# Kernel tuning notes

Measured on AMD Instinct MI355X. Metric: run time of the kernel, lower is better.

The kernel has to match this reference:

```python
import jax, jax.numpy as jnp
import numpy as np

N_E = 1024
E_DIM = 256
BETA = 0.25
PERSISTENCE = 0.1
B, T = 16, 1024


def setup_inputs() -> dict:
    key = jax.random.key(0)
    k1, k2 = jax.random.split(key)
    z = jax.random.normal(k1, (B, T, E_DIM), dtype=jnp.float32)
    # nn.Embedding(1+n_e, e_dim) init uniform(-1/n_e, 1/n_e)
    emb_weight = jax.random.uniform(k2, (N_E + 1, E_DIM), dtype=jnp.float32,
                                    minval=-1.0 / N_E, maxval=1.0 / N_E)
    return {"z": z, "emb_weight": emb_weight}


def _loss_contrast(z, ind, book):
    # z: (B,T,e), ind: (B,T) int, book: (n_e+1, e)
    z_q = book[ind]                                   # (B,T,e)
    loss_indices = jnp.sum((z - z_q) ** 2, axis=-1)   # (B,T)
    # ||z - book||^2 expanded to avoid the (B,T,n_e+1,e) intermediate
    z_sq = jnp.sum(z * z, axis=-1)                    # (B,T)
    b_sq = jnp.sum(book * book, axis=-1)              # (n_e+1,)
    cross = jnp.einsum('bte,ne->btn', z, book)        # (B,T,n_e+1)
    loss_all = z_sq[..., None] + b_sq[None, None, :] - 2.0 * cross
    lc = jnp.maximum(loss_indices[..., None] - loss_all + 1e-6 / N_E, 0.0)
    return jnp.mean(lc)


def _forward(z, emb_weight):
    zf = z.reshape(-1, E_DIM)
    d = (jnp.sum(zf * zf, axis=1, keepdims=True)
         + jnp.sum(emb_weight * emb_weight, axis=1)
         - 2.0 * (zf @ emb_weight.T)).reshape(B, T, N_E + 1)

    ind0 = jnp.clip(jnp.argmin(d[:, 0, :], axis=1), 0, N_E - 1)  # (B,)

    def step(carry, d_t):
        ind, coe = carry                              # (B,) int, (B,) f32
        d_here = jnp.take_along_axis(d_t, ind[:, None], axis=1)[:, 0]
        ind_next = jnp.minimum(ind + 1, N_E - 1)
        d_next = jnp.take_along_axis(d_t, ind_next[:, None], axis=1)[:, 0]
        stay = d_here <= d_next - coe
        ind_new = jnp.where(stay, ind, ind_next)
        coe_new = jnp.where(stay, coe + PERSISTENCE / N_E, 0.0)
        return (ind_new, coe_new), ind_new

    coe0 = jnp.zeros((B,), jnp.float32)
    _, inds = jax.lax.scan(step, (ind0, coe0), jnp.swapaxes(d[:, 1:, :], 0, 1))
    encoding_indices = jnp.concatenate([ind0[None, :], inds], axis=0).T  # (B,T)

    book_sg = jax.lax.stop_gradient(emb_weight)  # torch uses .data/.detach() everywhere
    z_q_raw = book_sg[encoding_indices]
    z_q = z + jax.lax.stop_gradient(z_q_raw - z)  # straight-through

    # non-legacy: beta * L(z, sg(book)) + L(sg(z), sg(book))
    loss = (BETA * _loss_contrast(z, encoding_indices, book_sg)
            + _loss_contrast(jax.lax.stop_gradient(z), encoding_indices, book_sg))

    v = jnp.max(encoding_indices) - jnp.min(encoding_indices)
    return z_q, loss, encoding_indices, v


def reference(z, emb_weight):
    return _forward(z, emb_weight)
```

## Files before the change

kernel.cpp:

```cpp
#include <hip/hip_runtime.h>

#define N_E   1024
#define EDIM  256
#define BB    16
#define TT    1024
#define NROW  (BB*TT)
#define NCOL  1025
#define NPAD  1152
#define PERS  (0.1f/1024.0f)
#define EPSC  (1e-6f/1024.0f)

#define OUT_LOSS 4194304
#define OUT_IDX  4194305
#define OUT_V    4210689

#define WS_ZB   0ull
#define WS_BBF  8388608ull
#define WS_BSQ  8978432ull
#define WS_E    8983552ull
#define WS_IND  84481024ull
#define WS_PART 84546560ull

typedef __attribute__((ext_vector_type(8))) short short8;
typedef __attribute__((ext_vector_type(4))) float floatx4;

__device__ __forceinline__ unsigned short f2bf(float f) {
    unsigned int u = __float_as_uint(f);
    u = (u + 0x7fffu + ((u >> 16) & 1u)) >> 16;
    return (unsigned short)u;
}

__device__ __forceinline__ float gload_f32(const float* p) {
    float r;
    asm volatile("global_load_dword %0, %1, off" : "=v"(r) : "v"(p));
    return r;
}

__global__ __launch_bounds__(256) void k0_prep(const float* __restrict__ z,
                                               const float* __restrict__ book,
                                               unsigned short* __restrict__ zb,
                                               unsigned short* __restrict__ bb,
                                               float* __restrict__ bsq) {
    int bx = blockIdx.x, tid = threadIdx.x;
    if (bx < 4096) {
        float4 v = ((const float4*)z)[bx * 256 + tid];
        size_t o = ((size_t)bx * 256 + tid) * 4;
        zb[o + 0] = f2bf(v.x); zb[o + 1] = f2bf(v.y);
        zb[o + 2] = f2bf(v.z); zb[o + 3] = f2bf(v.w);
    } else {
        int row = bx - 4096;
        float v = (row < NCOL) ? book[(size_t)row * EDIM + tid] : 0.0f;
        bb[(size_t)row * EDIM + tid] = f2bf(v);
        __shared__ float sd[256];
        sd[tid] = v * v;
        __syncthreads();
        for (int s = 128; s > 0; s >>= 1) { if (tid < s) sd[tid] += sd[tid + s]; __syncthreads(); }
        if (tid == 0) bsq[row] = sd[0];
    }
}

__global__ __launch_bounds__(256) void k1_gemm(const unsigned short* __restrict__ zb,
                                               const unsigned short* __restrict__ bb,
                                               const float* __restrict__ bsq,
                                               float* __restrict__ e) {
    int tid = threadIdx.x;
    int lane = tid & 63, w = tid >> 6;
    int mBase = blockIdx.x * 128 + (w >> 1) * 64;
    int nBase = blockIdx.y * 128 + (w & 1) * 64;
    int r = lane & 15, q = lane >> 4;

    floatx4 acc[4][4];
    #pragma unroll
    for (int i = 0; i < 4; i++)
        #pragma unroll
        for (int j = 0; j < 4; j++) acc[i][j] = (floatx4){0.f, 0.f, 0.f, 0.f};

    const short8* A = (const short8*)zb;
    const short8* Bm = (const short8*)bb;

    #pragma unroll
    for (int ks = 0; ks < 8; ks++) {
        int k8 = ks * 4 + q;
        short8 a[4], b[4];
        #pragma unroll
        for (int i = 0; i < 4; i++) a[i] = A[(size_t)(mBase + i * 16 + r) * 32 + k8];
        #pragma unroll
        for (int j = 0; j < 4; j++) b[j] = Bm[(size_t)(nBase + j * 16 + r) * 32 + k8];
        #pragma unroll
        for (int i = 0; i < 4; i++)
            #pragma unroll
            for (int j = 0; j < 4; j++)
                acc[i][j] = __builtin_amdgcn_mfma_f32_16x16x32_bf16(a[i], b[j], acc[i][j], 0, 0, 0);
    }

    float bsql[4];
    #pragma unroll
    for (int j = 0; j < 4; j++) bsql[j] = bsq[nBase + j * 16 + r];

    #pragma unroll
    for (int i = 0; i < 4; i++)
        #pragma unroll
        for (int rr = 0; rr < 4; rr++) {
            int m = mBase + i * 16 + q * 4 + rr;
            float* erow = e + (size_t)m * NPAD;
            #pragma unroll
            for (int j = 0; j < 4; j++)
                erow[nBase + j * 16 + r] = fmaf(-2.0f, acc[i][j][rr], bsql[j]);
        }
}


#define GCH 6

#define DECLW float A0_0, A0_1, A0_2, A1_0, A1_1, A1_2, \
                    A2_0, A2_1, A2_2, A3_0, A3_1, A3_2; \
              int q_0, q_1, q_2;

#define LDOP(S,k) { int _t = ti + 2*k + _g; _t = _t < 1024 ? _t : 1023; \
                    A##S##_##k = gload_f32(_pe + (size_t)_t * NPAD); }
#define LDSET0 LDOP(0,0) LDOP(0,1) LDOP(0,2)
#define LDSET1 LDOP(1,0) LDOP(1,1) LDOP(1,2)
#define LDSET2 LDOP(2,0) LDOP(2,1) LDOP(2,2)
#define LDSET3 LDOP(3,0) LDOP(3,1) LDOP(3,2)

#define QCOP(S,k) { float _bv = __shfl_down(A##S##_##k, 1, 32); \
                    int _qv = (int)((_bv - A##S##_##k) * QS); \
                    q_##k = _capn ? 0 : _qv; }
#define QCSET0 QCOP(0,0) QCOP(0,1) QCOP(0,2)
#define QCSET1 QCOP(1,0) QCOP(1,1) QCOP(1,2)
#define QCSET2 QCOP(2,0) QCOP(2,1) QCOP(2,2)
#define QCSET3 QCOP(3,0) QCOP(3,1) QCOP(3,2)

#define CHS(j,k,h) { int _rel = ind - b0; \
                     int _qv = __builtin_amdgcn_readlane(q_##k, _rel + h); \
                     bool _stay = (kk <= _qv); \
                     int _ip1 = ind + 1; _ip1 = _ip1 < 1023 ? _ip1 : 1023; \
                     ind = _stay ? ind : _ip1; \
                     kk  = _stay ? kk + 1 : 0; \
                     packed = (lane == j) ? ind : packed; }
#define CHAIN6 CHS(0,0,0) CHS(1,0,32) CHS(2,1,0) CHS(3,1,32) CHS(4,2,0) CHS(5,2,32)

#define ITERX(SI, SQ) { \
    int cbI = ind < 992 ? ind : 992;                  \
    { const float* _pe = eb + cbI + _cl; int ti = t + 24; LDSET##SI } \
    __builtin_amdgcn_sched_barrier(0); \
    int packed = 0; \
    CHAIN6 \
    if (lane < GCH && t + lane < 1024) wind[ibase + t + lane] = packed; \
    __builtin_amdgcn_sched_barrier(0); \
    asm volatile("s_waitcnt vmcnt(13)" ::: "memory");  \
    __builtin_amdgcn_sched_barrier(0); \
    { bool _capn = (b1 + _cl == 1023); QCSET##SQ } \
    __builtin_amdgcn_sched_barrier(0); \
    b0 = b1; b1 = b2; b2 = b3; b3 = cbI; \
    t += GCH; }

__global__ __launch_bounds__(256, 1) void k2_scan(const float* __restrict__ z,
                                                  const float* __restrict__ book,
                                                  const float* __restrict__ bsq,
                                                  const float* __restrict__ e,
                                                  int* __restrict__ wind) {
    __shared__ float sb[4]; __shared__ int si[4];

    int b = blockIdx.x, tid = threadIdx.x;
    int lane = tid & 63, w = tid >> 6;

    const float4* zr = (const float4*)(z + (size_t)b * TT * EDIM);
    float4 zv = zr[lane];
    float s = zv.x * zv.x + zv.y * zv.y + zv.z * zv.z + zv.w * zv.w;
    #pragma unroll
    for (int off = 32; off; off >>= 1) s += __shfl_xor(s, off, 64);
    float zsq = s;

    float best = 3.4e38f; int bidx = 0;
    for (int wi = w; wi < 17; wi += 4) {
        int n = wi * 64 + lane;
        if (n < NCOL) {
            const float4* br = (const float4*)(book + (size_t)n * EDIM);
            float c0 = 0.f, c1 = 0.f, c2 = 0.f, c3 = 0.f;
            #pragma unroll 8
            for (int k = 0; k < 64; k++) {
                float4 bo = br[k]; float4 za = zr[k];
                c0 = fmaf(za.x, bo.x, c0); c1 = fmaf(za.y, bo.y, c1);
                c2 = fmaf(za.z, bo.z, c2); c3 = fmaf(za.w, bo.w, c3);
            }
            float cr = (c0 + c1) + (c2 + c3);
            float d0 = (zsq + bsq[n]) - 2.0f * cr;
            if (d0 < best || (d0 == best && n < bidx)) { best = d0; bidx = n; }
        }
    }
    #pragma unroll
    for (int off = 32; off; off >>= 1) {
        float ob = __shfl_xor(best, off, 64);
        int   oi = __shfl_xor(bidx, off, 64);
        if (ob < best || (ob == best && oi < bidx)) { best = ob; bidx = oi; }
    }
    if (lane == 0) { sb[w] = best; si[w] = bidx; }
    __syncthreads();
    if (w != 0) return;

    best = sb[0]; bidx = si[0];
    for (int i = 1; i < 4; i++) {
        float vv = sb[i]; int ii = si[i];
        if (vv < best || (vv == best && ii < bidx)) { best = vv; bidx = ii; }
    }

    int ind = min(bidx, N_E - 1);
    int kk = 0;
    size_t ibase = (size_t)b * TT;

    const float* eb = e + (size_t)b * TT * NPAD;
    const float QS = 1.0f / PERS;

    int _g = lane >> 5;
    int _cl = lane & 31;

    DECLW

    asm volatile("s_waitcnt vmcnt(0)" ::: "memory");
    __builtin_amdgcn_sched_barrier(0);

    int base0 = ind < 992 ? ind : 992;
    int b0 = base0, b1 = base0, b2 = base0, b3 = base0;

    { const float* _pe = eb + base0 + _cl; int ti = 1;  LDSET0 }
    if (lane == 0) *(volatile int*)(wind + ibase) = ind;
    { const float* _pe = eb + base0 + _cl; int ti = 7;  LDSET1 }
    if (lane == 0) *(volatile int*)(wind + ibase) = ind;
    { const float* _pe = eb + base0 + _cl; int ti = 13; LDSET2 }
    if (lane == 0) *(volatile int*)(wind + ibase) = ind;
    { const float* _pe = eb + base0 + _cl; int ti = 19; LDSET3 }
    if (lane == 0) *(volatile int*)(wind + ibase) = ind;
    __builtin_amdgcn_sched_barrier(0);
    asm volatile("s_waitcnt vmcnt(13)" ::: "memory");
    __builtin_amdgcn_sched_barrier(0);
    {
        bool _capn = (b0 + _cl == 1023);
        QCSET0
    }
    __builtin_amdgcn_sched_barrier(0);

    int t = 1;
    #pragma unroll 1
    for (int cc = 0; cc < 43; cc++) {
        ITERX(0, 1)
        ITERX(1, 2)
        ITERX(2, 3)
        ITERX(3, 0)
    }
}

__global__ __launch_bounds__(256) void k3_loss_zq(const float* __restrict__ e,
                                                  const int* __restrict__ wind,
                                                  const float* __restrict__ book,
                                                  float* __restrict__ part,
                                                  float* __restrict__ out) {
    int rIdx = blockIdx.x, tid = threadIdx.x;
    int ind = wind[rIdx];
    const float* er = e + (size_t)rIdx * NPAD;
    float eind = er[ind];
    float p = 0.0f;
    for (int n = tid; n < NCOL; n += 256) {
        float v = eind - er[n] + EPSC;
        p += v > 0.0f ? v : 0.0f;
    }
    __shared__ float sd[256];
    sd[tid] = p; __syncthreads();
    for (int s = 128; s > 0; s >>= 1) { if (tid < s) sd[tid] += sd[tid + s]; __syncthreads(); }
    if (tid == 0) { part[rIdx] = sd[0]; out[OUT_IDX + rIdx] = (float)ind; }
    out[(size_t)rIdx * 256 + tid] = book[(size_t)ind * EDIM + tid];
}

__global__ __launch_bounds__(256) void k4_final(const float* __restrict__ part,
                                                const int* __restrict__ wind,
                                                float* __restrict__ out) {
    int tid = threadIdx.x;
    float s = 0.0f;
    for (int i = tid; i < NROW; i += 256) s += part[i];
    __shared__ float sd[256];
    sd[tid] = s; __syncthreads();
    for (int st = 128; st > 0; st >>= 1) { if (tid < st) sd[tid] += sd[tid + st]; __syncthreads(); }
    if (tid == 0) {
        int mn = wind[0], mx = wind[TT - 1];
        for (int b = 1; b < BB; b++) {
            mn = min(mn, wind[(size_t)b * TT]);
            mx = max(mx, wind[(size_t)b * TT + TT - 1]);
        }
        out[OUT_LOSS] = 1.25f * sd[0] / ((float)NROW * (float)NCOL);
        out[OUT_V] = (float)(mx - mn);
    }
}

extern "C" void kernel_launch(void* const* d_in, const int* in_sizes, int n_in,
                              void* d_out, int out_size, void* d_ws, size_t ws_size,
                              hipStream_t stream) {
    const float* z    = (const float*)d_in[0];
    const float* book = (const float*)d_in[1];
    char* ws = (char*)d_ws;
    unsigned short* zb = (unsigned short*)(ws + WS_ZB);
    unsigned short* bb = (unsigned short*)(ws + WS_BBF);
    float* bsq  = (float*)(ws + WS_BSQ);
    float* e    = (float*)(ws + WS_E);
    int*   wind = (int*)(ws + WS_IND);
    float* part = (float*)(ws + WS_PART);
    float* out  = (float*)d_out;

    hipLaunchKernelGGL(k0_prep,    dim3(4096 + 1152), dim3(256), 0, stream, z, book, zb, bb, bsq);
    hipLaunchKernelGGL(k1_gemm,    dim3(128, 9),      dim3(256), 0, stream, zb, bb, bsq, e);
    hipLaunchKernelGGL(k2_scan,    dim3(16),          dim3(256), 0, stream, z, book, bsq, e, wind);
    hipLaunchKernelGGL(k3_loss_zq, dim3(16384),       dim3(256), 0, stream, e, wind, book, part, out);
    hipLaunchKernelGGL(k4_final,   dim3(1),           dim3(256), 0, stream, part, wind, out);
}
```

Measured before the change: 241.0 us.

## Tile distance matrix into 32-column blocks for coalesced scan loads

```diff
diff --git a/kernel.cpp b/kernel.cpp
--- a/kernel.cpp
+++ b/kernel.cpp
@@ -20,6 +20,8 @@
 #define WS_E    8983552ull
 #define WS_IND  84481024ull
 #define WS_PART 84546560ull
+
+#define CBSTR 32768u
 
 typedef __attribute__((ext_vector_type(8))) short short8;
 typedef __attribute__((ext_vector_type(4))) float floatx4;
@@ -102,57 +104,68 @@
         #pragma unroll
         for (int rr = 0; rr < 4; rr++) {
             int m = mBase + i * 16 + q * 4 + rr;
-            float* erow = e + (size_t)m * NPAD;
+            float* ebb = e + ((size_t)(m >> 10) * 36) * CBSTR + (size_t)(m & 1023) * 32;
             #pragma unroll
-            for (int j = 0; j < 4; j++)
-                erow[nBase + j * 16 + r] = fmaf(-2.0f, acc[i][j][rr], bsql[j]);
+            for (int j = 0; j < 4; j++) {
+                int cb = (nBase >> 5) + (j >> 1);
+                int cl = ((j & 1) << 4) + r;
+                ebb[(size_t)cb * CBSTR + cl] = fmaf(-2.0f, acc[i][j][rr], bsql[j]);
+            }
         }
 }
 
 
 #define GCH 6
 
-#define DECLW float A0_0, A0_1, A0_2, A1_0, A1_1, A1_2, \
-                    A2_0, A2_1, A2_2, A3_0, A3_1, A3_2; \
-              int q_0, q_1, q_2;
-
-#define LDOP(S,k) { int _t = ti + 2*k + _g; _t = _t < 1024 ? _t : 1023; \
-                    A##S##_##k = gload_f32(_pe + (size_t)_t * NPAD); }
-#define LDSET0 LDOP(0,0) LDOP(0,1) LDOP(0,2)
-#define LDSET1 LDOP(1,0) LDOP(1,1) LDOP(1,2)
-#define LDSET2 LDOP(2,0) LDOP(2,1) LDOP(2,2)
-#define LDSET3 LDOP(3,0) LDOP(3,1) LDOP(3,2)
-
-#define QCOP(S,k) { float _bv = __shfl_down(A##S##_##k, 1, 32); \
-                    int _qv = (int)((_bv - A##S##_##k) * QS); \
-                    q_##k = _capn ? 0 : _qv; }
-#define QCSET0 QCOP(0,0) QCOP(0,1) QCOP(0,2)
-#define QCSET1 QCOP(1,0) QCOP(1,1) QCOP(1,2)
-#define QCSET2 QCOP(2,0) QCOP(2,1) QCOP(2,2)
-#define QCSET3 QCOP(3,0) QCOP(3,1) QCOP(3,2)
+#define DECLW float A00_0, A00_1, A00_2, A01_0, A01_1, A01_2, \
+                    A10_0, A10_1, A10_2, A11_0, A11_1, A11_2, \
+                    A20_0, A20_1, A20_2, A21_0, A21_1, A21_2; \
+              int q0_0, q0_1, q0_2, q1_0, q1_1, q1_2;
+
+#define LD6(S) { \
+    const float* _pb = eb5 + (size_t)(cbI >> 5) * CBSTR + lane; \
+    { size_t _o = (size_t)(ti)     * 32; \
+      A##S##0_0 = gload_f32(_pb + _o); A##S##1_0 = gload_f32(_pb + CBSTR + _o); } \
+    { size_t _o = (size_t)(ti + 2) * 32; \
+      A##S##0_1 = gload_f32(_pb + _o); A##S##1_1 = gload_f32(_pb + CBSTR + _o); } \
+    { size_t _o = (size_t)(ti + 4) * 32; \
+      A##S##0_2 = gload_f32(_pb + _o); A##S##1_2 = gload_f32(_pb + CBSTR + _o); } }
+
+#define QCW(S,k) { \
+    float _bv0 = __shfl_down(A##S##0_##k, 1, 32); \
+    float _bx  = __shfl_up(A##S##1_##k, 31, 32);   \
+    _bv0 = (_cl == 31) ? _bx : _bv0; \
+    q0_##k = (int)((_bv0 - A##S##0_##k) * QS); \
+    float _bv1 = __shfl_down(A##S##1_##k, 1, 32); \
+    int _q1 = (int)((_bv1 - A##S##1_##k) * QS); \
+    q1_##k = _cap1 ? 0 : _q1; }
+#define QCSET(S) QCW(S,0) QCW(S,1) QCW(S,2)
 
 #define CHS(j,k,h) { int _rel = ind - b0; \
-                     int _qv = __builtin_amdgcn_readlane(q_##k, _rel + h); \
-                     bool _stay = (kk <= _qv); \
-                     int _ip1 = ind + 1; _ip1 = _ip1 < 1023 ? _ip1 : 1023; \
-                     ind = _stay ? ind : _ip1; \
-                     kk  = _stay ? kk + 1 : 0; \
-                     packed = (lane == j) ? ind : packed; }
+    int _la = h + (_rel & 31); \
+    int _qa = __builtin_amdgcn_readlane(q0_##k, _la); \
+    int _qb = __builtin_amdgcn_readlane(q1_##k, _la); \
+    int _qv = _rel < 32 ? _qa : _qb; \
+    bool _stay = (kk <= _qv); \
+    int _ip1 = ind + 1; _ip1 = _ip1 < 1023 ? _ip1 : 1023; \
+    ind = _stay ? ind : _ip1; \
+    kk  = _stay ? kk + 1 : 0; \
+    packed = (lane == j) ? ind : packed; }
 #define CHAIN6 CHS(0,0,0) CHS(1,0,32) CHS(2,1,0) CHS(3,1,32) CHS(4,2,0) CHS(5,2,32)
 
-#define ITERX(SI, SQ) { \
-    int cbI = ind < 992 ? ind : 992;                  \
-    { const float* _pe = eb + cbI + _cl; int ti = t + 24; LDSET##SI } \
+#define ITERX(S, SQ) { \
+    int cbI = ind < 960 ? (ind & ~31) : 960;    \
+    { int ti = t + 18; LD6(S) } \
     __builtin_amdgcn_sched_barrier(0); \
     int packed = 0; \
     CHAIN6 \
     if (lane < GCH && t + lane < 1024) wind[ibase + t + lane] = packed; \
     __builtin_amdgcn_sched_barrier(0); \
-    asm volatile("s_waitcnt vmcnt(13)" ::: "memory");  \
+    asm volatile("s_waitcnt vmcnt(15)" ::: "memory");  \
     __builtin_amdgcn_sched_barrier(0); \
-    { bool _capn = (b1 + _cl == 1023); QCSET##SQ } \
+    { bool _cap1 = (b1 + 32 + _cl == 1023); QCSET(SQ) } \
     __builtin_amdgcn_sched_barrier(0); \
-    b0 = b1; b1 = b2; b2 = b3; b3 = cbI; \
+    b0 = b1; b1 = b2; b2 = cbI; \
     t += GCH; }
 
 __global__ __launch_bounds__(256, 1) void k2_scan(const float* __restrict__ z,
@@ -209,10 +222,9 @@
     int kk = 0;
     size_t ibase = (size_t)b * TT;
 
-    const float* eb = e + (size_t)b * TT * NPAD;
+    const float* eb5 = e + ((size_t)b * 36) * CBSTR;
     const float QS = 1.0f / PERS;
 
-    int _g = lane >> 5;
     int _cl = lane & 31;
 
     DECLW
@@ -220,33 +232,30 @@
     asm volatile("s_waitcnt vmcnt(0)" ::: "memory");
     __builtin_amdgcn_sched_barrier(0);
 
-    int base0 = ind < 992 ? ind : 992;
-    int b0 = base0, b1 = base0, b2 = base0, b3 = base0;
-
-    { const float* _pe = eb + base0 + _cl; int ti = 1;  LDSET0 }
+    int B0 = ind < 960 ? (ind & ~31) : 960;
+    int b0 = B0, b1 = B0, b2 = B0;
+
+    { int cbI = B0; { int ti = 1;  LD6(0) } }
     if (lane == 0) *(volatile int*)(wind + ibase) = ind;
-    { const float* _pe = eb + base0 + _cl; int ti = 7;  LDSET1 }
+    { int cbI = B0; { int ti = 7;  LD6(1) } }
     if (lane == 0) *(volatile int*)(wind + ibase) = ind;
-    { const float* _pe = eb + base0 + _cl; int ti = 13; LDSET2 }
-    if (lane == 0) *(volatile int*)(wind + ibase) = ind;
-    { const float* _pe = eb + base0 + _cl; int ti = 19; LDSET3 }
+    { int cbI = B0; { int ti = 13; LD6(2) } }
     if (lane == 0) *(volatile int*)(wind + ibase) = ind;
     __builtin_amdgcn_sched_barrier(0);
-    asm volatile("s_waitcnt vmcnt(13)" ::: "memory");
+    asm volatile("s_waitcnt vmcnt(15)" ::: "memory");
     __builtin_amdgcn_sched_barrier(0);
     {
-        bool _capn = (b0 + _cl == 1023);
-        QCSET0
+        bool _cap1 = (b0 + 32 + _cl == 1023);
+        QCSET(0)
     }
     __builtin_amdgcn_sched_barrier(0);
 
     int t = 1;
     #pragma unroll 1
-    for (int cc = 0; cc < 43; cc++) {
+    for (int cc = 0; cc < 57; cc++) {
         ITERX(0, 1)
         ITERX(1, 2)
-        ITERX(2, 3)
-        ITERX(3, 0)
+        ITERX(2, 0)
     }
 }
 
@@ -257,11 +266,11 @@
                                                   float* __restrict__ out) {
     int rIdx = blockIdx.x, tid = threadIdx.x;
     int ind = wind[rIdx];
-    const float* er = e + (size_t)rIdx * NPAD;
-    float eind = er[ind];
+    const float* er5 = e + ((size_t)(rIdx >> 10) * 36) * CBSTR + (size_t)(rIdx & 1023) * 32;
+    float eind = er5[(size_t)(ind >> 5) * CBSTR + (ind & 31)];
     float p = 0.0f;
     for (int n = tid; n < NCOL; n += 256) {
-        float v = eind - er[n] + EPSC;
+        float v = eind - er5[(size_t)(n >> 5) * CBSTR + (n & 31)] + EPSC;
         p += v > 0.0f ? v : 0.0f;
     }
     __shared__ float sd[256];
```

Result: slower. 266.8 us (+10.7%).
